# Optimization experiments

Hardware: AMD Instinct MI355X
Metric: run time of the kernel (lower is better)

The kernel has to match this reference:

```python
import jax, jax.numpy as jnp
import numpy as np

B, L, D = 2, 2048, 2048
NUM_HEADS = 32
KV_GROUPS = 8
GROUP_SIZE = NUM_HEADS // KV_GROUPS  # 4
HEAD_DIM = D // NUM_HEADS            # 64


def _rope_tables(L, hd):
    # standard RoPE angle tables, duplicated across halves to width hd
    inv_freq = 1.0 / (10000.0 ** (np.arange(0, hd, 2, dtype=np.float32) / hd))
    ang = np.arange(L, dtype=np.float32)[:, None] * inv_freq[None, :]  # [L, hd/2]
    cos = np.concatenate([np.cos(ang), np.cos(ang)], axis=-1)
    sin = np.concatenate([np.sin(ang), np.sin(ang)], axis=-1)
    return jnp.asarray(cos), jnp.asarray(sin)


def setup_inputs() -> dict:
    key = jax.random.key(0)
    ks = jax.random.split(key, 6)
    x = jax.random.normal(ks[0], (B, L, D), dtype=jnp.float32)
    mask = jnp.triu(jnp.ones((L, L), dtype=bool), k=1)  # causal: True above diag
    cos, sin = _rope_tables(L, HEAD_DIM)
    s = 0.02
    Wq = jax.random.normal(ks[1], (D, D), dtype=jnp.float32) * s
    Wk = jax.random.normal(ks[2], (D, KV_GROUPS * HEAD_DIM), dtype=jnp.float32) * s
    Wv = jax.random.normal(ks[3], (D, KV_GROUPS * HEAD_DIM), dtype=jnp.float32) * s
    Wo = jax.random.normal(ks[4], (D, D), dtype=jnp.float32) * s
    bo = jnp.zeros((D,), dtype=jnp.float32)
    return {"x": x, "mask": mask, "cos": cos, "sin": sin,
            "Wq": Wq, "Wk": Wk, "Wv": Wv, "Wo": Wo, "bo": bo}


def _apply_rope(t, cos, sin):
    # t: [B, H, L, hd]
    hd = t.shape[-1]
    t1, t2 = t[..., : hd // 2], t[..., hd // 2:]
    rotated = jnp.concatenate([-t2, t1], axis=-1)
    return t * cos[None, None, :, :] + rotated * sin[None, None, :, :]


def reference(x, mask, cos, sin, Wq, Wk, Wv, Wo, bo):
    Bv, Lv, Dv = x.shape
    hd = HEAD_DIM
    q = (x @ Wq).reshape(Bv, Lv, NUM_HEADS, hd).transpose(0, 2, 1, 3)   # [B,H,L,hd]
    k = (x @ Wk).reshape(Bv, Lv, KV_GROUPS, hd).transpose(0, 2, 1, 3)   # [B,G,L,hd]
    v = (x @ Wv).reshape(Bv, Lv, KV_GROUPS, hd).transpose(0, 2, 1, 3)
    q = _apply_rope(q, cos, sin)
    k = _apply_rope(k, cos, sin)
    k = jnp.repeat(k, GROUP_SIZE, axis=1)  # [B,H,L,hd]
    v = jnp.repeat(v, GROUP_SIZE, axis=1)
    scores = jnp.einsum('bhqd,bhkd->bhqk', q, k) / jnp.sqrt(jnp.float32(hd))
    scores = jnp.where(mask[None, None, :, :], -jnp.inf, scores)
    attn = jax.nn.softmax(scores, axis=-1)
    out = jnp.einsum('bhqk,bhkd->bhqd', attn, v)         # [B,H,L,hd]
    out = out.transpose(0, 2, 1, 3).reshape(Bv, Lv, Dv)  # [B,L,D]
    return out @ Wo + bo
```

## Files before the change

### kernel.cpp

```cpp
#include <hip/hip_runtime.h>
#include <cstdint>

typedef unsigned short UST;
typedef __bf16 v8bf __attribute__((ext_vector_type(8)));
typedef float v4f __attribute__((ext_vector_type(4)));

static __device__ __forceinline__ UST f2b(float f) {
  union { float f; uint32_t u; } c; c.f = f;
  uint32_t u = c.u;
  u += 0x7fffu + ((u >> 16) & 1u);
  return (UST)(u >> 16);
}
static __device__ __forceinline__ float b2f(UST h) {
  union { uint32_t u; float f; } c; c.u = ((uint32_t)h) << 16;
  return c.f;
}
static __device__ __forceinline__ uint32_t cvtpk(float lo, float hi) {
  uint32_t r;
  asm("v_cvt_pk_bf16_f32 %0, %1, %2" : "=v"(r) : "v"(lo), "v"(hi));
  return r;
}
static __device__ __forceinline__ float fexp2(float x) {
  float r;
  asm("v_exp_f32 %0, %1" : "=v"(r) : "v"(x));
  return r;
}
template <int N>
static __device__ __forceinline__ void wait_vm() {
  asm volatile("s_waitcnt vmcnt(%0)" :: "i"(N));
}

static __device__ __forceinline__ void gl_lds16(const UST* g, UST* l) {
  __builtin_amdgcn_global_load_lds(
      (const __attribute__((address_space(1))) void*)g,
      (__attribute__((address_space(3))) void*)l, 16, 0, 0);
}

__global__ __launch_bounds__(256) void k_cast(const float* __restrict__ src,
                                              UST* __restrict__ dst) {
  size_t i = (size_t)blockIdx.x * 256 + threadIdx.x;
  const float4* s4 = reinterpret_cast<const float4*>(src) + 2 * i;
  float4 a = s4[0], b = s4[1];
  union { UST s[8]; uint4 v; } r;
  r.s[0] = f2b(a.x); r.s[1] = f2b(a.y); r.s[2] = f2b(a.z); r.s[3] = f2b(a.w);
  r.s[4] = f2b(b.x); r.s[5] = f2b(b.y); r.s[6] = f2b(b.z); r.s[7] = f2b(b.w);
  reinterpret_cast<uint4*>(dst)[i] = r.v;
}

__global__ __launch_bounds__(256) void k_castT(const float* __restrict__ W,
                                               UST* __restrict__ dst, int N, int K) {
  __shared__ float tile[32][33];
  int nt = blockIdx.x * 32, kt = blockIdx.y * 32;
  int tx = threadIdx.x, ty = threadIdx.y;
#pragma unroll
  for (int r = 0; r < 4; ++r)
    tile[ty + r * 8][tx] = W[(size_t)(kt + ty + r * 8) * N + nt + tx];
  __syncthreads();
#pragma unroll
  for (int r = 0; r < 4; ++r)
    dst[(size_t)(nt + ty + r * 8) * K + kt + tx] = f2b(tile[tx][ty + r * 8]);
}

template <int BM, int BN, int WM, int WN, int EPI>
__global__ __launch_bounds__(512, 2) void k_gemm2(const UST* __restrict__ A,
                                                  const UST* __restrict__ Bt,
                                                  void* __restrict__ Cv,
                                                  const float* __restrict__ bias,
                                                  int M, int N, int K, int ntn) {
  constexpr int WMR = BM / WM, WNR = BN / WN;
  constexpr int MF = WMR / 16, NF = WNR / 16, MH = MF / 2;
  constexpr int CA = BM / 128, CB = BN / 128;
  constexpr int NKEEP = 2 * CA + CB;
  constexpr int AELEMS = 4 * BM * 32;
  __shared__ __align__(16) UST lds[AELEMS + 4 * BN * 32];

  int tid = threadIdx.x, w = tid >> 6, lane = tid & 63;
  int lr = lane & 15, lg = lane >> 4;
  int wm = w / WN, wn = w % WN;

  int T = (int)gridDim.x;
  int q = T >> 3;
  int bid = (int)blockIdx.x;
  int swz = (bid & 7) * q + (bid >> 3);
  int mBlk = (swz / ntn) * BM, nBlk = (swz % ntn) * BN;

  v4f acc[MF][NF];
#pragma unroll
  for (int i = 0; i < MF; ++i)
#pragma unroll
    for (int j = 0; j < NF; ++j) acc[i][j] = (v4f){0.f, 0.f, 0.f, 0.f};

  int srow = tid >> 2, scol = (tid & 3) * 8;
  const UST* Abase = A + (size_t)(mBlk + srow) * K + scol;
  const UST* Bbase = Bt + (size_t)(nBlk + srow) * K + scol;
  int ldsW = w * 512;

  auto stageA = [&](int buf, int s, int kt) {
#pragma unroll
    for (int i = 0; i < CA; ++i)
      gl_lds16(Abase + (size_t)(i * 128) * K + kt * 64 + s * 32,
               &lds[(buf * 2 + s) * BM * 32 + i * 4096 + ldsW]);
  };
  auto stageB = [&](int buf, int s, int kt) {
#pragma unroll
    for (int i = 0; i < CB; ++i)
      gl_lds16(Bbase + (size_t)(i * 128) * K + kt * 64 + s * 32,
               &lds[AELEMS + (buf * 2 + s) * BN * 32 + i * 4096 + ldsW]);
  };
  auto ldA = [&](int buf, int s, int mh, int f) -> v8bf {
    int row = wm * WMR + mh * (WMR / 2) + f * 16 + lr;
    return *(const v8bf*)&lds[((buf * 2 + s) * BM + row) * 32 + lg * 8];
  };
  auto ldB = [&](int buf, int s, int nf) -> v8bf {
    int row = wn * WNR + nf * 16 + lr;
    return *(const v8bf*)&lds[AELEMS + ((buf * 2 + s) * BN + row) * 32 + lg * 8];
  };

  int NT = K >> 6;
  stageA(0, 0, 0); stageB(0, 0, 0); stageA(0, 1, 0); stageB(0, 1, 0);

  for (int kt = 0; kt < NT; ++kt) {
    int buf = kt & 1, nb = buf ^ 1;
    bool more = (kt + 1 < NT);
#pragma unroll
    for (int s = 0; s < 2; ++s) {
      if (more) {
        stageA(nb, s, kt + 1);
        wait_vm<NKEEP>();
      } else {
        if (s == 0) wait_vm<CA + CB>(); else wait_vm<0>();
      }
      __builtin_amdgcn_s_barrier();
      __builtin_amdgcn_sched_barrier(0);
      v8bf bfr[NF], afr[MH];
#pragma unroll
      for (int nf = 0; nf < NF; ++nf) bfr[nf] = ldB(buf, s, nf);
#pragma unroll
      for (int f = 0; f < MH; ++f) afr[f] = ldA(buf, s, 0, f);
      __builtin_amdgcn_s_setprio(1);
#pragma unroll
      for (int f = 0; f < MH; ++f)
#pragma unroll
        for (int nf = 0; nf < NF; ++nf)
          acc[f][nf] = __builtin_amdgcn_mfma_f32_16x16x32_bf16(afr[f], bfr[nf],
                                                               acc[f][nf], 0, 0, 0);
      __builtin_amdgcn_s_setprio(0);
      __builtin_amdgcn_s_barrier();
      if (more) stageB(nb, s, kt + 1);
      __builtin_amdgcn_s_barrier();
      __builtin_amdgcn_sched_barrier(0);
#pragma unroll
      for (int f = 0; f < MH; ++f) afr[f] = ldA(buf, s, 1, f);
      __builtin_amdgcn_s_setprio(1);
#pragma unroll
      for (int f = 0; f < MH; ++f)
#pragma unroll
        for (int nf = 0; nf < NF; ++nf)
          acc[MH + f][nf] = __builtin_amdgcn_mfma_f32_16x16x32_bf16(afr[f], bfr[nf],
                                                                    acc[MH + f][nf], 0, 0, 0);
      __builtin_amdgcn_s_setprio(0);
      __builtin_amdgcn_s_barrier();
    }
  }

  int row0 = mBlk + wm * WMR + lg * 4;
  int col0 = nBlk + wn * WNR + lr;
#pragma unroll
  for (int fm = 0; fm < MF; ++fm)
#pragma unroll
    for (int nf = 0; nf < NF; ++nf)
#pragma unroll
      for (int r = 0; r < 4; ++r) {
        int row = row0 + fm * 16 + r;
        int col = col0 + nf * 16;
        if constexpr (EPI == 0) {
          ((UST*)Cv)[(size_t)row * N + col] = f2b(acc[fm][nf][r]);
        } else {
          ((float*)Cv)[(size_t)row * N + col] = acc[fm][nf][r] + bias[col];
        }
      }
}

__global__ __launch_bounds__(256) void k_rope(const UST* __restrict__ qkv,
                                              const float* __restrict__ cosT,
                                              const float* __restrict__ sinT,
                                              UST* __restrict__ qh,
                                              UST* __restrict__ kh) {
  int idx = blockIdx.x * 256 + threadIdx.x;
  int d = idx & 31;
  int hh = (idx >> 5) % 40;
  int row = idx / 1280;
  int l = row & 2047, b = row >> 11;
  int col = (hh < 32) ? hh * 64 : 2048 + (hh - 32) * 64;
  float t1 = b2f(qkv[(size_t)row * 3072 + col + d]);
  float t2 = b2f(qkv[(size_t)row * 3072 + col + d + 32]);
  float c = cosT[l * 64 + d], s = sinT[l * 64 + d];
  float o1 = t1 * c - t2 * s;
  float o2 = t2 * c + t1 * s;
  if (hh < 32) {
    size_t base = (((size_t)b * 32 + hh) * 2048 + l) * 64 + d;
    qh[base] = f2b(o1 * 0.125f);
    qh[base + 32] = f2b(o2 * 0.125f);
  } else {
    size_t base = (((size_t)b * 8 + (hh - 32)) * 2048 + l) * 64 + d;
    kh[base] = f2b(o1);
    kh[base + 32] = f2b(o2);
  }
}

__global__ __launch_bounds__(256) void k_vtrans(const UST* __restrict__ qkv,
                                                UST* __restrict__ vt) {
  __shared__ __align__(16) UST tl[64][72];
  int lt = blockIdx.x, bg = blockIdx.y;
  int b = bg >> 3, g = bg & 7;
  int t = threadIdx.x;
  int li = t >> 2, d0 = (t & 3) * 16;
  const UST* src = qkv + (size_t)(b * 2048 + lt * 64 + li) * 3072 + 2560 + g * 64 + d0;
  *(uint4*)&tl[li][d0] = *(const uint4*)src;
  *(uint4*)&tl[li][d0 + 8] = *(const uint4*)(src + 8);
  __syncthreads();
  int d = t >> 2, l0 = (t & 3) * 16;
  union { UST u[8]; uint4 v; } r0, r1;
#pragma unroll
  for (int e = 0; e < 8; ++e) r0.u[e] = tl[l0 + e][d];
#pragma unroll
  for (int e = 0; e < 8; ++e) r1.u[e] = tl[l0 + 8 + e][d];
  UST* dstp = vt + (size_t)((b * 8 + g) * 64 + d) * 2048 + (size_t)lt * 64 + l0;
  *(uint4*)dstp = r0.v;
  *(uint4*)(dstp + 8) = r1.v;
}

__global__ __launch_bounds__(512, 4) void k_attn(const UST* __restrict__ qh,
                                                 const UST* __restrict__ kh,
                                                 const UST* __restrict__ vt,
                                                 UST* __restrict__ outp) {
  __shared__ __align__(16) UST k_s[128 * 72];
  __shared__ __align__(16) UST v_s[64 * 136];
  __shared__ __align__(16) UST p_s[8][16 * 136];
  int bx = blockIdx.x, h = blockIdx.y, b = blockIdx.z;
  int g = h >> 2;
  int tid = threadIdx.x, w = tid >> 6, lane = tid & 63;
  int lr = lane & 15, lg = lane >> 4;

  int ksr = tid >> 2, ksc = (tid & 3) * 16;
  int vsr = tid >> 3, vsc = (tid & 7) * 16;
  const UST* kbase = kh + ((size_t)(b * 8 + g) * 2048 + ksr) * 64 + ksc;
  const UST* vbase = vt + ((size_t)(b * 8 + g) * 64 + vsr) * 2048 + vsc;
  UST* kdst = &k_s[ksr * 72 + ksc];
  UST* vdst = &v_s[vsr * 136 + vsc];

  for (int half = 0; half < 2; ++half) {
    int qt = half ? (15 - bx) : bx;
    int qbase = qt * 128 + w * 16;

    const UST* qp = qh + ((size_t)(b * 32 + h) * 2048 + qbase + lr) * 64 + lg * 8;
    v8bf qf0 = *(const v8bf*)qp;
    v8bf qf1 = *(const v8bf*)(qp + 32);

    float m = -1e30f, ls = 0.f;
    v4f o[4];
#pragma unroll
    for (int dt = 0; dt < 4; ++dt) o[dt] = (v4f){0.f, 0.f, 0.f, 0.f};

    __syncthreads();
    uint4 pk0 = *(const uint4*)kbase, pk1 = *(const uint4*)(kbase + 8);
    uint4 pv0 = *(const uint4*)vbase, pv1 = *(const uint4*)(vbase + 8);
    *(uint4*)kdst = pk0; *(uint4*)(kdst + 8) = pk1;
    *(uint4*)vdst = pv0; *(uint4*)(vdst + 8) = pv1;

    for (int j = 0; j <= qt; ++j) {
      __syncthreads();
      bool pref = (j < qt);
      if (pref) {
        const UST* kg = kbase + (size_t)(j + 1) * 8192;
        const UST* vg = vbase + (j + 1) * 128;
        pk0 = *(const uint4*)kg; pk1 = *(const uint4*)(kg + 8);
        pv0 = *(const uint4*)vg; pv1 = *(const uint4*)(vg + 8);
      }

      v4f st[8];
      __builtin_amdgcn_s_setprio(1);
#pragma unroll
      for (int kt = 0; kt < 8; ++kt) {
        const UST* kr = &k_s[(kt * 16 + lr) * 72 + lg * 8];
        v8bf kf0 = *(const v8bf*)kr;
        v8bf kf1 = *(const v8bf*)(kr + 32);
        v4f z = (v4f){0.f, 0.f, 0.f, 0.f};
        z = __builtin_amdgcn_mfma_f32_16x16x32_bf16(kf0, qf0, z, 0, 0, 0);
        z = __builtin_amdgcn_mfma_f32_16x16x32_bf16(kf1, qf1, z, 0, 0, 0);
        st[kt] = z;
      }
      __builtin_amdgcn_s_setprio(0);
      if (j == qt) {
        int qg = qbase + lr;
#pragma unroll
        for (int kt = 0; kt < 8; ++kt)
#pragma unroll
          for (int r = 0; r < 4; ++r) {
            int kg2 = j * 128 + kt * 16 + 4 * lg + r;
            if (kg2 > qg) st[kt][r] = -1e30f;
          }
      }

      float t0 = fmaxf(fmaxf(st[0][0], st[0][1]), fmaxf(st[0][2], st[0][3]));
      float t1 = fmaxf(fmaxf(st[1][0], st[1][1]), fmaxf(st[1][2], st[1][3]));
      float t2 = fmaxf(fmaxf(st[2][0], st[2][1]), fmaxf(st[2][2], st[2][3]));
      float t3 = fmaxf(fmaxf(st[3][0], st[3][1]), fmaxf(st[3][2], st[3][3]));
      float t4 = fmaxf(fmaxf(st[4][0], st[4][1]), fmaxf(st[4][2], st[4][3]));
      float t5 = fmaxf(fmaxf(st[5][0], st[5][1]), fmaxf(st[5][2], st[5][3]));
      float t6 = fmaxf(fmaxf(st[6][0], st[6][1]), fmaxf(st[6][2], st[6][3]));
      float t7 = fmaxf(fmaxf(st[7][0], st[7][1]), fmaxf(st[7][2], st[7][3]));
      float mx = fmaxf(fmaxf(fmaxf(t0, t1), fmaxf(t2, t3)),
                       fmaxf(fmaxf(t4, t5), fmaxf(t6, t7)));
      mx = fmaxf(mx, __shfl_xor(mx, 16));
      mx = fmaxf(mx, __shfl_xor(mx, 32));

      if (!__all(mx <= m + 8.f)) {
        float mn = fmaxf(m, mx);
        float al = __expf(m - mn);
        m = mn;
        ls *= al;
#pragma unroll
        for (int r = 0; r < 4; ++r) {
          float ar = __shfl(al, 4 * lg + r);
          o[0][r] *= ar; o[1][r] *= ar; o[2][r] *= ar; o[3][r] *= ar;
        }
      }

      constexpr float LOG2E = 1.44269504f;
      float mlog = m * LOG2E;
      float rs = 0.f;
      UST* pw = &p_s[w][lr * 136 + 4 * lg];
#pragma unroll
      for (int kt = 0; kt < 8; ++kt) {
        float p0 = fexp2(__builtin_fmaf(st[kt][0], LOG2E, -mlog));
        float p1 = fexp2(__builtin_fmaf(st[kt][1], LOG2E, -mlog));
        float p2 = fexp2(__builtin_fmaf(st[kt][2], LOG2E, -mlog));
        float p3 = fexp2(__builtin_fmaf(st[kt][3], LOG2E, -mlog));
        rs += (p0 + p1) + (p2 + p3);
        uint2 q2;
        q2.x = cvtpk(p0, p1);
        q2.y = cvtpk(p2, p3);
        *(uint2*)(pw + kt * 16) = q2;
      }
      rs += __shfl_xor(rs, 16);
      rs += __shfl_xor(rs, 32);
      ls += rs;

      __builtin_amdgcn_s_setprio(1);
#pragma unroll
      for (int kk = 0; kk < 4; ++kk) {
        v8bf pa = *(const v8bf*)&p_s[w][lr * 136 + kk * 32 + lg * 8];
#pragma unroll
        for (int dt = 0; dt < 4; ++dt) {
          v8bf vb = *(const v8bf*)&v_s[(dt * 16 + lr) * 136 + kk * 32 + lg * 8];
          o[dt] = __builtin_amdgcn_mfma_f32_16x16x32_bf16(pa, vb, o[dt], 0, 0, 0);
        }
      }
      __builtin_amdgcn_s_setprio(0);

      __syncthreads();
      if (pref) {
        *(uint4*)kdst = pk0; *(uint4*)(kdst + 8) = pk1;
        *(uint4*)vdst = pv0; *(uint4*)(vdst + 8) = pv1;
      }
    }

    float iv = 1.f / ls;
#pragma unroll
    for (int r = 0; r < 4; ++r) {
      float ivr = __shfl(iv, 4 * lg + r);
      size_t rowb = ((size_t)b * 2048 + qbase + 4 * lg + r) * 2048 + h * 64 + lr;
#pragma unroll
      for (int dt = 0; dt < 4; ++dt)
        outp[rowb + dt * 16] = f2b(o[dt][r] * ivr);
    }
  }
}

extern "C" void kernel_launch(void* const* d_in, const int* in_sizes, int n_in,
                              void* d_out, int out_size, void* d_ws, size_t ws_size,
                              hipStream_t stream) {
  const float* x    = (const float*)d_in[0];
  const float* cosT = (const float*)d_in[2];
  const float* sinT = (const float*)d_in[3];
  const float* Wq   = (const float*)d_in[4];
  const float* Wk   = (const float*)d_in[5];
  const float* Wv   = (const float*)d_in[6];
  const float* Wo   = (const float*)d_in[7];
  const float* bo   = (const float*)d_in[8];
  float* out = (float*)d_out;

  char* ws = (char*)d_ws;
  UST* xb   = (UST*)(ws);
  UST* wcat = (UST*)(ws + 16777216);
  UST* wot  = (UST*)(ws + 29360128);
  UST* qkv  = (UST*)(ws + 37748736);
  UST* qhp  = (UST*)(ws + 62914560);
  UST* khp  = (UST*)(ws + 79691776);
  UST* vtp  = (UST*)(ws + 83886080);
  UST* attn_o = xb;

  k_cast<<<4096, 256, 0, stream>>>(x, xb);
  k_castT<<<dim3(64, 64), dim3(32, 8), 0, stream>>>(Wq, wcat, 2048, 2048);
  k_castT<<<dim3(16, 64), dim3(32, 8), 0, stream>>>(Wk, wcat + (size_t)2048 * 2048, 512, 2048);
  k_castT<<<dim3(16, 64), dim3(32, 8), 0, stream>>>(Wv, wcat + (size_t)2560 * 2048, 512, 2048);
  k_castT<<<dim3(64, 64), dim3(32, 8), 0, stream>>>(Wo, wot, 2048, 2048);

  k_gemm2<256, 256, 2, 4, 0><<<192, 512, 0, stream>>>(xb, wcat, qkv, nullptr,
                                                      4096, 3072, 2048, 12);
  k_rope<<<20480, 256, 0, stream>>>(qkv, cosT, sinT, qhp, khp);
  k_vtrans<<<dim3(32, 16), 256, 0, stream>>>(qkv, vtp);
  k_attn<<<dim3(8, 32, 2), 512, 0, stream>>>(qhp, khp, vtp, attn_o);
  k_gemm2<256, 128, 4, 2, 1><<<256, 512, 0, stream>>>(attn_o, wot, out, bo,
                                                      4096, 2048, 2048, 16);
}
```

Baseline: 219.6 us.

## Retile QKV GEMM to 256x192 and restructure GEMM prefetch/barrier pipeline

The QKV projection GEMM changes from 256x256 tiles on 192 blocks to 256x192 tiles on 256 blocks, so the grid fills all 256 CUs. B staging gains a partial-chunk path because 192 is not a multiple of 128. The main loop is regrouped so fragment loads come before the next tile's global->LDS prefetch, with one wait and barrier per half. The output GEMM uses a single M-half with all prefetches issued together. This risks different wait counts and more register pressure in the single-half path.

```diff
diff --git a/kernel.cpp b/kernel.cpp
--- a/kernel.cpp
+++ b/kernel.cpp
@@ -61,16 +61,17 @@
     dst[(size_t)(nt + ty + r * 8) * K + kt + tx] = f2b(tile[tx][ty + r * 8]);
 }
 
-template <int BM, int BN, int WM, int WN, int EPI>
+template <int BM, int BN, int WM, int WN, int NMH, int EPI>
 __global__ __launch_bounds__(512, 2) void k_gemm2(const UST* __restrict__ A,
                                                   const UST* __restrict__ Bt,
                                                   void* __restrict__ Cv,
                                                   const float* __restrict__ bias,
                                                   int M, int N, int K, int ntn) {
   constexpr int WMR = BM / WM, WNR = BN / WN;
-  constexpr int MF = WMR / 16, NF = WNR / 16, MH = MF / 2;
-  constexpr int CA = BM / 128, CB = BN / 128;
-  constexpr int NKEEP = 2 * CA + CB;
+  constexpr int MF = WMR / 16, NF = WNR / 16, MH = MF / NMH;
+  constexpr int CA = BM / 128;
+  constexpr int CBF = BN / 128;
+  constexpr int BREM = (BN % 128) / 64;
   constexpr int AELEMS = 4 * BM * 32;
   __shared__ __align__(16) UST lds[AELEMS + 4 * BN * 32];
 
@@ -78,8 +79,7 @@
   int lr = lane & 15, lg = lane >> 4;
   int wm = w / WN, wn = w % WN;
 
-  int T = (int)gridDim.x;
-  int q = T >> 3;
+  int q = (int)gridDim.x >> 3;
   int bid = (int)blockIdx.x;
   int swz = (bid & 7) * q + (bid >> 3);
   int mBlk = (swz / ntn) * BM, nBlk = (swz % ntn) * BN;
@@ -103,12 +103,25 @@
   };
   auto stageB = [&](int buf, int s, int kt) {
 #pragma unroll
-    for (int i = 0; i < CB; ++i)
+    for (int i = 0; i < CBF; ++i)
       gl_lds16(Bbase + (size_t)(i * 128) * K + kt * 64 + s * 32,
                &lds[AELEMS + (buf * 2 + s) * BN * 32 + i * 4096 + ldsW]);
+    if constexpr (BREM) {
+      if (w < 4)
+        gl_lds16(Bbase + (size_t)(CBF * 128) * K + kt * 64 + s * 32,
+                 &lds[AELEMS + (buf * 2 + s) * BN * 32 + CBF * 4096 + ldsW]);
+    }
   };
-  auto ldA = [&](int buf, int s, int mh, int f) -> v8bf {
-    int row = wm * WMR + mh * (WMR / 2) + f * 16 + lr;
+  auto waitNK = [&]() {
+    if constexpr (BREM) {
+      if (w < 4) wait_vm<CA + CBF + 1>();
+      else       wait_vm<CA + CBF>();
+    } else {
+      wait_vm<CA + CBF>();
+    }
+  };
+  auto ldA = [&](int buf, int s, int f) -> v8bf {
+    int row = wm * WMR + f * 16 + lr;
     return *(const v8bf*)&lds[((buf * 2 + s) * BM + row) * 32 + lg * 8];
   };
   auto ldB = [&](int buf, int s, int nf) -> v8bf {
@@ -118,48 +131,46 @@
 
   int NT = K >> 6;
   stageA(0, 0, 0); stageB(0, 0, 0); stageA(0, 1, 0); stageB(0, 1, 0);
+  waitNK();
+  __builtin_amdgcn_s_barrier();
 
   for (int kt = 0; kt < NT; ++kt) {
     int buf = kt & 1, nb = buf ^ 1;
     bool more = (kt + 1 < NT);
 #pragma unroll
     for (int s = 0; s < 2; ++s) {
-      if (more) {
-        stageA(nb, s, kt + 1);
-        wait_vm<NKEEP>();
-      } else {
-        if (s == 0) wait_vm<CA + CB>(); else wait_vm<0>();
-      }
-      __builtin_amdgcn_s_barrier();
-      __builtin_amdgcn_sched_barrier(0);
-      v8bf bfr[NF], afr[MH];
-#pragma unroll
-      for (int nf = 0; nf < NF; ++nf) bfr[nf] = ldB(buf, s, nf);
-#pragma unroll
-      for (int f = 0; f < MH; ++f) afr[f] = ldA(buf, s, 0, f);
-      __builtin_amdgcn_s_setprio(1);
-#pragma unroll
-      for (int f = 0; f < MH; ++f)
-#pragma unroll
-        for (int nf = 0; nf < NF; ++nf)
-          acc[f][nf] = __builtin_amdgcn_mfma_f32_16x16x32_bf16(afr[f], bfr[nf],
-                                                               acc[f][nf], 0, 0, 0);
-      __builtin_amdgcn_s_setprio(0);
-      __builtin_amdgcn_s_barrier();
-      if (more) stageB(nb, s, kt + 1);
-      __builtin_amdgcn_s_barrier();
-      __builtin_amdgcn_sched_barrier(0);
-#pragma unroll
-      for (int f = 0; f < MH; ++f) afr[f] = ldA(buf, s, 1, f);
-      __builtin_amdgcn_s_setprio(1);
-#pragma unroll
-      for (int f = 0; f < MH; ++f)
-#pragma unroll
-        for (int nf = 0; nf < NF; ++nf)
-          acc[MH + f][nf] = __builtin_amdgcn_mfma_f32_16x16x32_bf16(afr[f], bfr[nf],
-                                                                    acc[MH + f][nf], 0, 0, 0);
-      __builtin_amdgcn_s_setprio(0);
-      __builtin_amdgcn_s_barrier();
+      v8bf bfr[NF];
+#pragma unroll
+      for (int mh = 0; mh < NMH; ++mh) {
+        v8bf afr[MH];
+        if (mh == 0) {
+#pragma unroll
+          for (int nf = 0; nf < NF; ++nf) bfr[nf] = ldB(buf, s, nf);
+        }
+#pragma unroll
+        for (int f = 0; f < MH; ++f) afr[f] = ldA(buf, s, mh * MH + f);
+        if constexpr (NMH == 2) {
+          if (mh == 0) {
+            if (more) stageA(nb, s, kt + 1);
+          } else {
+            if (more) { stageB(nb, s, kt + 1); waitNK(); }
+            else if (s == 0) wait_vm<0>();
+          }
+        } else {
+          if (more) { stageA(nb, s, kt + 1); stageB(nb, s, kt + 1); waitNK(); }
+          else if (s == 0) wait_vm<0>();
+        }
+        __builtin_amdgcn_s_barrier();
+        __builtin_amdgcn_s_setprio(1);
+#pragma unroll
+        for (int f = 0; f < MH; ++f)
+#pragma unroll
+          for (int nf = 0; nf < NF; ++nf)
+            acc[mh * MH + f][nf] = __builtin_amdgcn_mfma_f32_16x16x32_bf16(
+                afr[f], bfr[nf], acc[mh * MH + f][nf], 0, 0, 0);
+        __builtin_amdgcn_s_setprio(0);
+        __builtin_amdgcn_s_barrier();
+      }
     }
   }
 
@@ -407,11 +418,11 @@
   k_castT<<<dim3(16, 64), dim3(32, 8), 0, stream>>>(Wv, wcat + (size_t)2560 * 2048, 512, 2048);
   k_castT<<<dim3(64, 64), dim3(32, 8), 0, stream>>>(Wo, wot, 2048, 2048);
 
-  k_gemm2<256, 256, 2, 4, 0><<<192, 512, 0, stream>>>(xb, wcat, qkv, nullptr,
-                                                      4096, 3072, 2048, 12);
+  k_gemm2<256, 192, 2, 4, 2, 0><<<256, 512, 0, stream>>>(xb, wcat, qkv, nullptr,
+                                                         4096, 3072, 2048, 16);
   k_rope<<<20480, 256, 0, stream>>>(qkv, cosT, sinT, qhp, khp);
   k_vtrans<<<dim3(32, 16), 256, 0, stream>>>(qkv, vtp);
   k_attn<<<dim3(8, 32, 2), 512, 0, stream>>>(qhp, khp, vtp, attn_o);
-  k_gemm2<256, 128, 4, 2, 1><<<256, 512, 0, stream>>>(attn_o, wot, out, bo,
-                                                      4096, 2048, 2048, 16);
-}
+  k_gemm2<256, 128, 4, 2, 1, 1><<<256, 512, 0, stream>>>(attn_o, wot, out, bo,
+                                                         4096, 2048, 2048, 16);
+}
```

After: 206.1 us. -6.2%, faster.

## Restructure GEMM LDS staging with XOR-swizzled 64-wide K tiles and retile QKV GEMM

Applied to the files above, without the earlier changes.

The bf16 GEMM now stages full 64-wide K slices per buffer into LDS, using an XOR swizzle on the 16-byte column groups to avoid bank conflicts. This replaces the split half-tile schedule and its multiple s_barriers with a simpler double-buffered loop that has two __syncthreads per iteration. The QKV projection is retiled from 256x256 over 192 blocks to 256x192 over 256 blocks, giving more even coverage of the compute units. The cost is less interleaving of loads with MFMA work and more barrier stalls per K step.

```diff
diff --git a/kernel.cpp b/kernel.cpp
--- a/kernel.cpp
+++ b/kernel.cpp
@@ -68,18 +68,17 @@
                                                   const float* __restrict__ bias,
                                                   int M, int N, int K, int ntn) {
   constexpr int WMR = BM / WM, WNR = BN / WN;
-  constexpr int MF = WMR / 16, NF = WNR / 16, MH = MF / 2;
-  constexpr int CA = BM / 128, CB = BN / 128;
-  constexpr int NKEEP = 2 * CA + CB;
-  constexpr int AELEMS = 4 * BM * 32;
-  __shared__ __align__(16) UST lds[AELEMS + 4 * BN * 32];
+  constexpr int MF = WMR / 16, NF = WNR / 16;
+  constexpr int CA = BM / 64, CB = BN / 64;
+  constexpr int NKEEP = CA + CB;
+  constexpr int AE = 2 * BM * 64;
+  __shared__ __align__(16) UST lds[AE + 2 * BN * 64];
 
   int tid = threadIdx.x, w = tid >> 6, lane = tid & 63;
   int lr = lane & 15, lg = lane >> 4;
   int wm = w / WN, wn = w % WN;
 
-  int T = (int)gridDim.x;
-  int q = T >> 3;
+  int q = (int)gridDim.x >> 3;
   int bid = (int)blockIdx.x;
   int swz = (bid & 7) * q + (bid >> 3);
   int mBlk = (swz / ntn) * BM, nBlk = (swz % ntn) * BN;
@@ -90,77 +89,62 @@
 #pragma unroll
     for (int j = 0; j < NF; ++j) acc[i][j] = (v4f){0.f, 0.f, 0.f, 0.f};
 
-  int srow = tid >> 2, scol = (tid & 3) * 8;
-  const UST* Abase = A + (size_t)(mBlk + srow) * K + scol;
-  const UST* Bbase = Bt + (size_t)(nBlk + srow) * K + scol;
+  int tr = tid >> 3;
+  int sg = (tid & 7) ^ (tr & 7);
+  const UST* AbL = A + (size_t)(mBlk + tr) * K + sg * 8;
+  const UST* BbL = Bt + (size_t)(nBlk + tr) * K + sg * 8;
   int ldsW = w * 512;
 
-  auto stageA = [&](int buf, int s, int kt) {
-#pragma unroll
-    for (int i = 0; i < CA; ++i)
-      gl_lds16(Abase + (size_t)(i * 128) * K + kt * 64 + s * 32,
-               &lds[(buf * 2 + s) * BM * 32 + i * 4096 + ldsW]);
+  auto stageA = [&](int bf, int kt) {
+#pragma unroll
+    for (int c = 0; c < CA; ++c)
+      gl_lds16(AbL + (size_t)(c * 64) * K + kt * 64,
+               &lds[bf * BM * 64 + c * 4096 + ldsW]);
   };
-  auto stageB = [&](int buf, int s, int kt) {
-#pragma unroll
-    for (int i = 0; i < CB; ++i)
-      gl_lds16(Bbase + (size_t)(i * 128) * K + kt * 64 + s * 32,
-               &lds[AELEMS + (buf * 2 + s) * BN * 32 + i * 4096 + ldsW]);
+  auto stageB = [&](int bf, int kt) {
+#pragma unroll
+    for (int c = 0; c < CB; ++c)
+      gl_lds16(BbL + (size_t)(c * 64) * K + kt * 64,
+               &lds[AE + bf * BN * 64 + c * 4096 + ldsW]);
   };
-  auto ldA = [&](int buf, int s, int mh, int f) -> v8bf {
-    int row = wm * WMR + mh * (WMR / 2) + f * 16 + lr;
-    return *(const v8bf*)&lds[((buf * 2 + s) * BM + row) * 32 + lg * 8];
+  auto ldA = [&](int bf, int s, int f) -> v8bf {
+    int row = wm * WMR + f * 16 + lr;
+    return *(const v8bf*)&lds[(bf * BM + row) * 64 + (((s * 4 + lg) ^ (lr & 7)) * 8)];
   };
-  auto ldB = [&](int buf, int s, int nf) -> v8bf {
+  auto ldB = [&](int bf, int s, int nf) -> v8bf {
     int row = wn * WNR + nf * 16 + lr;
-    return *(const v8bf*)&lds[AELEMS + ((buf * 2 + s) * BN + row) * 32 + lg * 8];
+    return *(const v8bf*)&lds[AE + (bf * BN + row) * 64 + (((s * 4 + lg) ^ (lr & 7)) * 8)];
   };
 
   int NT = K >> 6;
-  stageA(0, 0, 0); stageB(0, 0, 0); stageA(0, 1, 0); stageB(0, 1, 0);
+  stageA(0, 0); stageB(0, 0);
 
   for (int kt = 0; kt < NT; ++kt) {
-    int buf = kt & 1, nb = buf ^ 1;
-    bool more = (kt + 1 < NT);
+    int bf = kt & 1, nb = bf ^ 1;
+    if (kt + 1 < NT) {
+      stageA(nb, kt + 1); stageB(nb, kt + 1);
+      wait_vm<NKEEP>();
+    } else {
+      wait_vm<0>();
+    }
+    __syncthreads();
 #pragma unroll
     for (int s = 0; s < 2; ++s) {
-      if (more) {
-        stageA(nb, s, kt + 1);
-        wait_vm<NKEEP>();
-      } else {
-        if (s == 0) wait_vm<CA + CB>(); else wait_vm<0>();
-      }
-      __builtin_amdgcn_s_barrier();
-      __builtin_amdgcn_sched_barrier(0);
-      v8bf bfr[NF], afr[MH];
-#pragma unroll
-      for (int nf = 0; nf < NF; ++nf) bfr[nf] = ldB(buf, s, nf);
-#pragma unroll
-      for (int f = 0; f < MH; ++f) afr[f] = ldA(buf, s, 0, f);
+      v8bf afr[MF], bfr[NF];
+#pragma unroll
+      for (int nf = 0; nf < NF; ++nf) bfr[nf] = ldB(bf, s, nf);
+#pragma unroll
+      for (int f = 0; f < MF; ++f) afr[f] = ldA(bf, s, f);
       __builtin_amdgcn_s_setprio(1);
 #pragma unroll
-      for (int f = 0; f < MH; ++f)
+      for (int f = 0; f < MF; ++f)
 #pragma unroll
         for (int nf = 0; nf < NF; ++nf)
-          acc[f][nf] = __builtin_amdgcn_mfma_f32_16x16x32_bf16(afr[f], bfr[nf],
-                                                               acc[f][nf], 0, 0, 0);
+          acc[f][nf] = __builtin_amdgcn_mfma_f32_16x16x32_bf16(
+              afr[f], bfr[nf], acc[f][nf], 0, 0, 0);
       __builtin_amdgcn_s_setprio(0);
-      __builtin_amdgcn_s_barrier();
-      if (more) stageB(nb, s, kt + 1);
-      __builtin_amdgcn_s_barrier();
-      __builtin_amdgcn_sched_barrier(0);
-#pragma unroll
-      for (int f = 0; f < MH; ++f) afr[f] = ldA(buf, s, 1, f);
-      __builtin_amdgcn_s_setprio(1);
-#pragma unroll
-      for (int f = 0; f < MH; ++f)
-#pragma unroll
-        for (int nf = 0; nf < NF; ++nf)
-          acc[MH + f][nf] = __builtin_amdgcn_mfma_f32_16x16x32_bf16(afr[f], bfr[nf],
-                                                                    acc[MH + f][nf], 0, 0, 0);
-      __builtin_amdgcn_s_setprio(0);
-      __builtin_amdgcn_s_barrier();
     }
+    __syncthreads();
   }
 
   int row0 = mBlk + wm * WMR + lg * 4;
@@ -407,8 +391,8 @@
   k_castT<<<dim3(16, 64), dim3(32, 8), 0, stream>>>(Wv, wcat + (size_t)2560 * 2048, 512, 2048);
   k_castT<<<dim3(64, 64), dim3(32, 8), 0, stream>>>(Wo, wot, 2048, 2048);
 
-  k_gemm2<256, 256, 2, 4, 0><<<192, 512, 0, stream>>>(xb, wcat, qkv, nullptr,
-                                                      4096, 3072, 2048, 12);
+  k_gemm2<256, 192, 2, 4, 0><<<256, 512, 0, stream>>>(xb, wcat, qkv, nullptr,
+                                                      4096, 3072, 2048, 16);
   k_rope<<<20480, 256, 0, stream>>>(qkv, cosT, sinT, qhp, khp);
   k_vtrans<<<dim3(32, 16), 256, 0, stream>>>(qkv, vtp);
   k_attn<<<dim3(8, 32, 2), 512, 0, stream>>>(qhp, khp, vtp, attn_o);
```

New measurement: 218.5 us. No clear change (-0.5%).
